# Kernel optimization log

Hardware: AMD Instinct MI355X
Metric: run time of the kernel (lower is better)

Reference implementation:

```python
import jax, jax.numpy as jnp
import numpy as np

B, S, D = 2, 4096, 2048
HQ, HK, HV = 32, 8, 8
H = max(HQ, HK, HV)
DK, DV = 64, 64
OUT = 2048
CHUNK = 64  # chunked-recurrent block size


def setup_inputs() -> dict:
    key = jax.random.key(0)
    k1, k2, k3 = jax.random.split(key, 3)
    x = jax.random.normal(k1, (B, S, D), dtype=jnp.float32)
    input_state = jnp.zeros((B, H * DK * DV), dtype=jnp.float32)
    qkv = HQ * DK + HK * DK + HV * DV  # 3072
    # Linear weights stored as [in, out]; equals torch weight.T so y = x @ W
    W_in = jax.random.normal(k2, (D, qkv), dtype=jnp.float32) * (D ** -0.5)
    W_out = jax.random.normal(k3, (H * DV, OUT), dtype=jnp.float32) * ((H * DV) ** -0.5)
    return {"x": x, "input_state": input_state, "W_in": W_in, "W_out": W_out}


def _linear_attention(q, k, v, S0):
    # q,k,v: [B,S,H,d]; S0: [B,H,DK,DV]
    nc = S // CHUNK
    # move chunk axis to front for lax.scan: [nc, B, CHUNK, H, d]
    qc = jnp.moveaxis(q.reshape(B, nc, CHUNK, H, DK), 1, 0)
    kc = jnp.moveaxis(k.reshape(B, nc, CHUNK, H, DK), 1, 0)
    vc = jnp.moveaxis(v.reshape(B, nc, CHUNK, H, DV), 1, 0)
    mask = jnp.tril(jnp.ones((CHUNK, CHUNK), dtype=bool))  # causal within chunk

    def step(Sstate, blk):
        qb, kb, vb = blk  # [B,C,H,d]
        A = jnp.einsum('bihd,bjhd->bhij', qb, kb)
        A = jnp.where(mask, A, jnp.zeros((), A.dtype))
        o = jnp.einsum('bhij,bjhd->bihd', A, vb) \
            + jnp.einsum('bihd,bhde->bihe', qb, Sstate)
        Sstate = Sstate + jnp.einsum('bjhd,bjhe->bhde', kb, vb)
        return Sstate, o

    Sf, o = jax.lax.scan(step, S0, (qc, kc, vc))
    o = jnp.moveaxis(o, 0, 1).reshape(B, S, H, DV)
    return o, Sf


def reference(x, input_state, W_in, W_out):
    proj = x @ W_in  # [B,S,3072]
    q, k, v = jnp.split(proj, [HQ * DK, HQ * DK + HK * DK], axis=-1)
    q = q.reshape(B, S, HQ, DK)
    k = k.reshape(B, S, HK, DK)
    v = v.reshape(B, S, HV, DV)
    # GQA: repeat kv heads up to num_heads = max(...)
    k = jnp.repeat(k, H // HK, axis=2)
    v = jnp.repeat(v, H // HV, axis=2)
    S0 = input_state.reshape(B, H, DK, DV)
    o, Sf = _linear_attention(q, k, v, S0)
    out = o.reshape(B, S, H * DV) @ W_out
    return out, Sf.reshape(B, H, DK * DV)
```

## Files before the change

kernel.cpp:

```cpp
#include <hip/hip_runtime.h>

typedef __bf16 bf16_t;
typedef __bf16 bf16x8 __attribute__((ext_vector_type(8)));
typedef __bf16 bf16x4 __attribute__((ext_vector_type(4)));
typedef float  f32x4  __attribute__((ext_vector_type(4)));

#define MFMA16(a,b,c) __builtin_amdgcn_mfma_f32_16x16x32_bf16((a),(b),(c),0,0,0)

__device__ __forceinline__ void gl_lds16(const void* g, void* l) {
    __builtin_amdgcn_global_load_lds(
        (__attribute__((address_space(1))) void*)(g),
        (__attribute__((address_space(3))) void*)(l),
        16, 0, 0);
}

static constexpr int S_TOT   = 8192;
static constexpr int D_IN    = 2048;
static constexpr int QKV     = 3072;
static constexpr int OUT_D   = 2048;
static constexpr int NCHUNK  = 64;

__global__ __launch_bounds__(256)
void cvt_f32_bf16(const float* __restrict__ in, bf16_t* __restrict__ out) {
    int i = blockIdx.x * 256 + threadIdx.x;
    f32x4 v = ((const f32x4*)in)[i];
    bf16x4 o;
    o[0] = (bf16_t)v[0]; o[1] = (bf16_t)v[1]; o[2] = (bf16_t)v[2]; o[3] = (bf16_t)v[3];
    ((bf16x4*)out)[i] = o;
}

__global__ __launch_bounds__(256)
void transpose_f32_bf16(const float* __restrict__ in, bf16_t* __restrict__ out, int R, int C) {
    __shared__ float tile[64][65];
    const int t  = threadIdx.x;
    const int r0 = blockIdx.y * 64, c0 = blockIdx.x * 64;
#pragma unroll
    for (int p = 0; p < 4; p++) {
        int row = p * 16 + (t >> 4);
        int col = (t & 15) * 4;
        f32x4 v = *(const f32x4*)&in[(size_t)(r0 + row) * C + c0 + col];
        tile[row][col + 0] = v[0]; tile[row][col + 1] = v[1];
        tile[row][col + 2] = v[2]; tile[row][col + 3] = v[3];
    }
    __syncthreads();
#pragma unroll
    for (int p = 0; p < 4; p++) {
        int oc  = p * 16 + (t >> 4);
        int orr = (t & 15) * 4;
        bf16x4 v;
        v[0] = (bf16_t)tile[orr + 0][oc]; v[1] = (bf16_t)tile[orr + 1][oc];
        v[2] = (bf16_t)tile[orr + 2][oc]; v[3] = (bf16_t)tile[orr + 3][oc];
        *(bf16x4*)&out[(size_t)(c0 + oc) * R + r0 + orr] = v;
    }
}

template<int OUT_BF16>
__global__ __launch_bounds__(256, 4)
void gemm_bt(const bf16_t* __restrict__ A, const bf16_t* __restrict__ Bt,
             void* __restrict__ Cout, int M, int N, int K) {
    __shared__ alignas(16) bf16_t lA[128 * 32];
    __shared__ alignas(16) bf16_t lB[128 * 32];
    const int tid = threadIdx.x;
    const int m0 = blockIdx.y * 128;
    const int n0 = blockIdx.x * 128;
    const int w = tid >> 6, lane = tid & 63;
    const int wr = (w >> 1) * 64, wc = (w & 1) * 64;
    const int l15 = lane & 15, q8 = (lane >> 4) * 8, q4 = (lane >> 4) * 4;
    f32x4 acc[4][4] = {};
    const bf16_t* Ag = A + (size_t)(m0 + (tid >> 2)) * K + (tid & 3) * 8;
    const bf16_t* Bg = Bt + (size_t)(n0 + (tid >> 2)) * K + (tid & 3) * 8;
    const size_t rowStep = (size_t)64 * K;
    bf16_t* lA_t = lA + tid * 8;
    bf16_t* lB_t = lB + tid * 8;
    for (int k0 = 0; k0 < K; k0 += 32) {
        gl_lds16(Ag + k0,           lA_t);
        gl_lds16(Ag + k0 + rowStep, lA_t + 64 * 32);
        gl_lds16(Bg + k0,           lB_t);
        gl_lds16(Bg + k0 + rowStep, lB_t + 64 * 32);
        __syncthreads();
        bf16x8 bfr[4];
#pragma unroll
        for (int nj = 0; nj < 4; nj++) bfr[nj] = *(const bf16x8*)&lB[(wc + nj * 16 + l15) * 32 + q8];
#pragma unroll
        for (int mi = 0; mi < 4; mi++) {
            bf16x8 afr = *(const bf16x8*)&lA[(wr + mi * 16 + l15) * 32 + q8];
#pragma unroll
            for (int nj = 0; nj < 4; nj++)
                acc[mi][nj] = MFMA16(afr, bfr[nj], acc[mi][nj]);
        }
        __syncthreads();
    }
    if (OUT_BF16) {
        bf16_t* C = (bf16_t*)Cout;
#pragma unroll
        for (int mi = 0; mi < 4; mi++)
#pragma unroll
            for (int nj = 0; nj < 4; nj++)
#pragma unroll
                for (int r = 0; r < 4; r++)
                    C[(size_t)(m0 + wr + mi * 16 + q4 + r) * N + n0 + wc + nj * 16 + l15] =
                        (bf16_t)acc[mi][nj][r];
    } else {
        float* C = (float*)Cout;
#pragma unroll
        for (int mi = 0; mi < 4; mi++)
#pragma unroll
            for (int nj = 0; nj < 4; nj++)
#pragma unroll
                for (int r = 0; r < 4; r++)
                    C[(size_t)(m0 + wr + mi * 16 + q4 + r) * N + n0 + wc + nj * 16 + l15] =
                        acc[mi][nj][r];
    }
}

__global__ __launch_bounds__(64)
void transpose_kv(const bf16_t* __restrict__ proj,
                  bf16_t* __restrict__ kT_g, bf16_t* __restrict__ vT_g) {
    const int idx = blockIdx.x;
    const int c = idx & 63, hk = (idx >> 6) & 7, b = idx >> 9;
    const int tokBase = b * 4096 + c * 64;
    __shared__ float tile[64][65];
    const int lane = threadIdx.x;
#pragma unroll
    for (int which = 0; which < 2; which++) {
        const bf16_t* src = proj + (size_t)tokBase * QKV + 2048 + which * 512 + hk * 64;
        bf16_t* dst = (which ? vT_g : kT_g) + (size_t)idx * 4096;
#pragma unroll
        for (int p = 0; p < 8; p++) {
            int tok = p * 8 + (lane >> 3);
            int d0  = (lane & 7) * 8;
            bf16x8 v = *(const bf16x8*)&src[(size_t)tok * QKV + d0];
#pragma unroll
            for (int e = 0; e < 8; e++) tile[tok][d0 + e] = (float)v[e];
        }
        __syncthreads();
#pragma unroll
        for (int p = 0; p < 8; p++) {
            int dk = p * 8 + (lane >> 3);
            int t0 = (lane & 7) * 8;
            bf16x8 o;
#pragma unroll
            for (int e = 0; e < 8; e++) o[e] = (bf16_t)tile[t0 + e][dk];
            *(bf16x8*)&dst[dk * 64 + t0] = o;
        }
        __syncthreads();
    }
}

__global__ __launch_bounds__(64)
void chunk_kv(const bf16_t* __restrict__ kT_g, const bf16_t* __restrict__ vT_g,
              float* __restrict__ Zc) {
    const int idx = blockIdx.x;
    const int lane = threadIdx.x;
    const int l15 = lane & 15, q8 = (lane >> 4) * 8, q4 = (lane >> 4) * 4;
    const bf16_t* vT = vT_g + (size_t)idx * 4096;
    const bf16_t* kT = kT_g + (size_t)idx * 4096;
    f32x4 acc[4][4] = {};
#pragma unroll
    for (int ks = 0; ks < 2; ks++) {
        bf16x8 af[4], bf_[4];
#pragma unroll
        for (int mi = 0; mi < 4; mi++) af[mi]  = *(const bf16x8*)&vT[(mi * 16 + l15) * 64 + ks * 32 + q8];
#pragma unroll
        for (int nj = 0; nj < 4; nj++) bf_[nj] = *(const bf16x8*)&kT[(nj * 16 + l15) * 64 + ks * 32 + q8];
#pragma unroll
        for (int mi = 0; mi < 4; mi++)
#pragma unroll
            for (int nj = 0; nj < 4; nj++)
                acc[mi][nj] = MFMA16(af[mi], bf_[nj], acc[mi][nj]);
    }
    float* zout = Zc + (size_t)idx * 4096;
#pragma unroll
    for (int mi = 0; mi < 4; mi++)
#pragma unroll
        for (int nj = 0; nj < 4; nj++)
#pragma unroll
            for (int r = 0; r < 4; r++)
                zout[(mi * 16 + q4 + r) * 64 + nj * 16 + l15] = acc[mi][nj][r];
}

__global__ __launch_bounds__(256)
void prefix_state(const float* __restrict__ Zc, const float* __restrict__ S0,
                  bf16_t* __restrict__ Zp, float* __restrict__ SfOut) {
    const int slice = blockIdx.x & 15;
    const int bh = blockIdx.x >> 4;
    const int h = bh & 31, b = bh >> 5;
    const int hk = h >> 2;
    const int e = slice * 256 + threadIdx.x;
    const int dv = e >> 6, dk = e & 63;
    float acc = S0[(size_t)b * 131072 + h * 4096 + dk * 64 + dv];
    const float* zc = Zc + ((size_t)(b * 8 + hk) * 64) * 4096 + e;
    bf16_t* zp = Zp + ((size_t)(b * 32 + h) * 64) * 4096 + e;
    for (int c = 0; c < NCHUNK; c++) {
        zp[(size_t)c * 4096] = (bf16_t)acc;
        acc += zc[(size_t)c * 4096];
    }
    SfOut[(size_t)b * 131072 + h * 4096 + dk * 64 + dv] = acc;
}

__global__ __launch_bounds__(64)
void attn_chunk(const bf16_t* __restrict__ proj, const bf16_t* __restrict__ vT_g,
                const bf16_t* __restrict__ Zp, bf16_t* __restrict__ O) {
    const int idx = blockIdx.x;
    const int g = idx & 3, hk = (idx >> 2) & 7, c = (idx >> 5) & 63, b = idx >> 11;
    const int h = hk * 4 + g;
    const int tokBase = b * 4096 + c * 64;
    __shared__ alignas(16) bf16_t zs[64 * 64];
    const int lane = threadIdx.x;
    const int l15 = lane & 15, q8 = (lane >> 4) * 8, q4 = (lane >> 4) * 4;
    const bf16_t* qrow  = proj + (size_t)tokBase * QKV + h * 64;
    const bf16_t* krow  = proj + (size_t)tokBase * QKV + 2048 + hk * 64;
    const bf16_t* zrow  = Zp + (((size_t)(b * 32 + h)) * 64 + c) * 4096;
    const bf16_t* vTrow = vT_g + ((size_t)(b * 8 + hk) * 64 + c) * 4096;

    bf16x8 qf[2][4];
#pragma unroll
    for (int ks = 0; ks < 2; ks++)
#pragma unroll
        for (int mi = 0; mi < 4; mi++)
            qf[ks][mi] = *(const bf16x8*)&qrow[(size_t)(mi * 16 + l15) * QKV + ks * 32 + q8];

    f32x4 oacc[4][4] = {};
#pragma unroll
    for (int ks = 0; ks < 2; ks++) {
        bf16x8 zf[4];
#pragma unroll
        for (int nj = 0; nj < 4; nj++) zf[nj] = *(const bf16x8*)&zrow[(nj * 16 + l15) * 64 + ks * 32 + q8];
#pragma unroll
        for (int mi = 0; mi < 4; mi++)
#pragma unroll
            for (int nj = 0; nj < 4; nj++)
                oacc[mi][nj] = MFMA16(qf[ks][mi], zf[nj], oacc[mi][nj]);
    }
    f32x4 sacc[4][4] = {};
#pragma unroll
    for (int ks = 0; ks < 2; ks++) {
        bf16x8 kf[4];
#pragma unroll
        for (int nj = 0; nj < 4; nj++) kf[nj] = *(const bf16x8*)&krow[(size_t)(nj * 16 + l15) * QKV + ks * 32 + q8];
#pragma unroll
        for (int mi = 0; mi < 4; mi++)
#pragma unroll
            for (int nj = 0; nj < 4; nj++)
                if (mi >= nj) sacc[mi][nj] = MFMA16(qf[ks][mi], kf[nj], sacc[mi][nj]);
    }
#pragma unroll
    for (int mi = 0; mi < 4; mi++)
#pragma unroll
        for (int nj = 0; nj < 4; nj++)
#pragma unroll
            for (int r = 0; r < 4; r++) {
                int ti = mi * 16 + q4 + r, tj = nj * 16 + l15;
                float v = (ti >= tj) ? sacc[mi][nj][r] : 0.0f;
                zs[ti * 64 + tj] = (bf16_t)v;
            }
    __syncthreads();
#pragma unroll
    for (int ks = 0; ks < 2; ks++) {
        bf16x8 sf[4], vf[4];
#pragma unroll
        for (int mi = 0; mi < 4; mi++) sf[mi] = *(const bf16x8*)&zs[(mi * 16 + l15) * 64 + ks * 32 + q8];
#pragma unroll
        for (int nj = 0; nj < 4; nj++) vf[nj] = *(const bf16x8*)&vTrow[(nj * 16 + l15) * 64 + ks * 32 + q8];
#pragma unroll
        for (int mi = 0; mi < 4; mi++)
#pragma unroll
            for (int nj = 0; nj < 4; nj++)
                oacc[mi][nj] = MFMA16(sf[mi], vf[nj], oacc[mi][nj]);
    }
    bf16_t* og = O + (size_t)tokBase * OUT_D + h * 64;
#pragma unroll
    for (int mi = 0; mi < 4; mi++)
#pragma unroll
        for (int nj = 0; nj < 4; nj++)
#pragma unroll
            for (int r = 0; r < 4; r++)
                og[(size_t)(mi * 16 + q4 + r) * OUT_D + nj * 16 + l15] = (bf16_t)oacc[mi][nj][r];
}

extern "C" void kernel_launch(void* const* d_in, const int* in_sizes, int n_in,
                              void* d_out, int out_size, void* d_ws, size_t ws_size,
                              hipStream_t stream) {
    const float* x     = (const float*)d_in[0];
    const float* S0    = (const float*)d_in[1];
    const float* W_in  = (const float*)d_in[2];
    const float* W_out = (const float*)d_in[3];

    char* ws = (char*)d_ws;
    bf16_t* xb    = (bf16_t*)(ws + 0);
    bf16_t* kT_g  = (bf16_t*)(ws + 16777216);
    bf16_t* WinT  = (bf16_t*)(ws + 33554432);
    bf16_t* vT_g  = (bf16_t*)(ws + 33554432);
    bf16_t* WoutT = (bf16_t*)(ws + 46137344);
    bf16_t* proj  = (bf16_t*)(ws + 54525952);
    float*  Zc    = (float*) (ws + 104857600);
    bf16_t* Zp    = (bf16_t*)(ws + 121634816);
    bf16_t* Ob    = (bf16_t*)(ws + 0);

    float* outMain  = (float*)d_out;
    float* outState = (float*)d_out + (size_t)S_TOT * OUT_D;

    cvt_f32_bf16<<<16384, 256, 0, stream>>>(x, xb);
    transpose_f32_bf16<<<dim3(48, 32), 256, 0, stream>>>(W_in, WinT, 2048, 3072);
    transpose_f32_bf16<<<dim3(32, 32), 256, 0, stream>>>(W_out, WoutT, 2048, 2048);
    gemm_bt<1><<<dim3(24, 64), 256, 0, stream>>>(xb, WinT, proj, S_TOT, QKV, D_IN);
    transpose_kv<<<1024, 64, 0, stream>>>(proj, kT_g, vT_g);
    chunk_kv<<<1024, 64, 0, stream>>>(kT_g, vT_g, Zc);
    prefix_state<<<1024, 256, 0, stream>>>(Zc, S0, Zp, outState);
    attn_chunk<<<4096, 64, 0, stream>>>(proj, vT_g, Zp, Ob);
    gemm_bt<0><<<dim3(16, 64), 256, 0, stream>>>(Ob, WoutT, outMain, S_TOT, OUT_D, OUT_D);
}
```

Before: 414.4 us.

## Fuse prep kernels, merge kv transpose with chunk state, regroup attention heads

Several changes land together. The three conversion and transpose kernels become one launch. The K/V transpose is fused with the per-chunk KᵀV computation, reading K directly from shared memory and dropping the kT buffer. The attention kernel now runs the four GQA query heads of a KV head as four warps in one 256-thread block, with a padded shared-memory stride to cut bank conflicts. The input GEMM processes two N tiles per block with half the grid. The intent is to reduce launch count, global traffic and LDS conflicts. The risks are lower GEMM parallelism and more LDS usage per block.

```diff
diff --git a/kernel.cpp b/kernel.cpp
--- a/kernel.cpp
+++ b/kernel.cpp
@@ -19,21 +19,28 @@
 static constexpr int QKV     = 3072;
 static constexpr int OUT_D   = 2048;
 static constexpr int NCHUNK  = 64;
+static constexpr int ZSTR    = 88;
 
 __global__ __launch_bounds__(256)
-void cvt_f32_bf16(const float* __restrict__ in, bf16_t* __restrict__ out) {
-    int i = blockIdx.x * 256 + threadIdx.x;
-    f32x4 v = ((const f32x4*)in)[i];
-    bf16x4 o;
-    o[0] = (bf16_t)v[0]; o[1] = (bf16_t)v[1]; o[2] = (bf16_t)v[2]; o[3] = (bf16_t)v[3];
-    ((bf16x4*)out)[i] = o;
-}
-
-__global__ __launch_bounds__(256)
-void transpose_f32_bf16(const float* __restrict__ in, bf16_t* __restrict__ out, int R, int C) {
+void prep(const float* __restrict__ x, bf16_t* __restrict__ xb,
+          const float* __restrict__ W_in, bf16_t* __restrict__ WinT,
+          const float* __restrict__ W_out, bf16_t* __restrict__ WoutT) {
     __shared__ float tile[64][65];
-    const int t  = threadIdx.x;
-    const int r0 = blockIdx.y * 64, c0 = blockIdx.x * 64;
+    const int bid = blockIdx.x;
+    const int t   = threadIdx.x;
+    if (bid < 16384) {
+        int i = bid * 256 + t;
+        f32x4 v = ((const f32x4*)x)[i];
+        bf16x4 o;
+        o[0] = (bf16_t)v[0]; o[1] = (bf16_t)v[1]; o[2] = (bf16_t)v[2]; o[3] = (bf16_t)v[3];
+        ((bf16x4*)xb)[i] = o;
+        return;
+    }
+    const float* in; bf16_t* out; int R, C, bx, by;
+    int tb = bid - 16384;
+    if (tb < 1536) { in = W_in;  out = WinT;  R = 2048; C = 3072; bx = tb % 48; by = tb / 48; }
+    else { tb -= 1536; in = W_out; out = WoutT; R = 2048; C = 2048; bx = tb % 32; by = tb / 32; }
+    const int r0 = by * 64, c0 = bx * 64;
 #pragma unroll
     for (int p = 0; p < 4; p++) {
         int row = p * 16 + (t >> 4);
@@ -54,7 +61,7 @@
     }
 }
 
-template<int OUT_BF16>
+template<int OUT_BF16, int NTILE, int NSTRIDE>
 __global__ __launch_bounds__(256, 4)
 void gemm_bt(const bf16_t* __restrict__ A, const bf16_t* __restrict__ Bt,
              void* __restrict__ Cout, int M, int N, int K) {
@@ -62,107 +69,106 @@
     __shared__ alignas(16) bf16_t lB[128 * 32];
     const int tid = threadIdx.x;
     const int m0 = blockIdx.y * 128;
-    const int n0 = blockIdx.x * 128;
     const int w = tid >> 6, lane = tid & 63;
     const int wr = (w >> 1) * 64, wc = (w & 1) * 64;
     const int l15 = lane & 15, q8 = (lane >> 4) * 8, q4 = (lane >> 4) * 4;
-    f32x4 acc[4][4] = {};
     const bf16_t* Ag = A + (size_t)(m0 + (tid >> 2)) * K + (tid & 3) * 8;
-    const bf16_t* Bg = Bt + (size_t)(n0 + (tid >> 2)) * K + (tid & 3) * 8;
     const size_t rowStep = (size_t)64 * K;
     bf16_t* lA_t = lA + tid * 8;
     bf16_t* lB_t = lB + tid * 8;
-    for (int k0 = 0; k0 < K; k0 += 32) {
-        gl_lds16(Ag + k0,           lA_t);
-        gl_lds16(Ag + k0 + rowStep, lA_t + 64 * 32);
-        gl_lds16(Bg + k0,           lB_t);
-        gl_lds16(Bg + k0 + rowStep, lB_t + 64 * 32);
-        __syncthreads();
-        bf16x8 bfr[4];
-#pragma unroll
-        for (int nj = 0; nj < 4; nj++) bfr[nj] = *(const bf16x8*)&lB[(wc + nj * 16 + l15) * 32 + q8];
-#pragma unroll
-        for (int mi = 0; mi < 4; mi++) {
-            bf16x8 afr = *(const bf16x8*)&lA[(wr + mi * 16 + l15) * 32 + q8];
-#pragma unroll
-            for (int nj = 0; nj < 4; nj++)
-                acc[mi][nj] = MFMA16(afr, bfr[nj], acc[mi][nj]);
+#pragma unroll
+    for (int tI = 0; tI < NTILE; tI++) {
+        const int n0 = (blockIdx.x + tI * NSTRIDE) * 128;
+        const bf16_t* Bg = Bt + (size_t)(n0 + (tid >> 2)) * K + (tid & 3) * 8;
+        f32x4 acc[4][4] = {};
+        for (int k0 = 0; k0 < K; k0 += 32) {
+            gl_lds16(Ag + k0,           lA_t);
+            gl_lds16(Ag + k0 + rowStep, lA_t + 64 * 32);
+            gl_lds16(Bg + k0,           lB_t);
+            gl_lds16(Bg + k0 + rowStep, lB_t + 64 * 32);
+            __syncthreads();
+            bf16x8 bfr[4];
+#pragma unroll
+            for (int nj = 0; nj < 4; nj++) bfr[nj] = *(const bf16x8*)&lB[(wc + nj * 16 + l15) * 32 + q8];
+#pragma unroll
+            for (int mi = 0; mi < 4; mi++) {
+                bf16x8 afr = *(const bf16x8*)&lA[(wr + mi * 16 + l15) * 32 + q8];
+#pragma unroll
+                for (int nj = 0; nj < 4; nj++)
+                    acc[mi][nj] = MFMA16(afr, bfr[nj], acc[mi][nj]);
+            }
+            __syncthreads();
         }
-        __syncthreads();
-    }
-    if (OUT_BF16) {
-        bf16_t* C = (bf16_t*)Cout;
-#pragma unroll
-        for (int mi = 0; mi < 4; mi++)
-#pragma unroll
-            for (int nj = 0; nj < 4; nj++)
-#pragma unroll
-                for (int r = 0; r < 4; r++)
-                    C[(size_t)(m0 + wr + mi * 16 + q4 + r) * N + n0 + wc + nj * 16 + l15] =
-                        (bf16_t)acc[mi][nj][r];
-    } else {
-        float* C = (float*)Cout;
-#pragma unroll
-        for (int mi = 0; mi < 4; mi++)
-#pragma unroll
-            for (int nj = 0; nj < 4; nj++)
-#pragma unroll
-                for (int r = 0; r < 4; r++)
-                    C[(size_t)(m0 + wr + mi * 16 + q4 + r) * N + n0 + wc + nj * 16 + l15] =
-                        acc[mi][nj][r];
+        if (OUT_BF16) {
+            bf16_t* C = (bf16_t*)Cout;
+#pragma unroll
+            for (int mi = 0; mi < 4; mi++)
+#pragma unroll
+                for (int nj = 0; nj < 4; nj++)
+#pragma unroll
+                    for (int r = 0; r < 4; r++)
+                        C[(size_t)(m0 + wr + mi * 16 + q4 + r) * N + n0 + wc + nj * 16 + l15] =
+                            (bf16_t)acc[mi][nj][r];
+        } else {
+            float* C = (float*)Cout;
+#pragma unroll
+            for (int mi = 0; mi < 4; mi++)
+#pragma unroll
+                for (int nj = 0; nj < 4; nj++)
+#pragma unroll
+                    for (int r = 0; r < 4; r++)
+                        C[(size_t)(m0 + wr + mi * 16 + q4 + r) * N + n0 + wc + nj * 16 + l15] =
+                            acc[mi][nj][r];
+        }
     }
 }
 
 __global__ __launch_bounds__(64)
-void transpose_kv(const bf16_t* __restrict__ proj,
-                  bf16_t* __restrict__ kT_g, bf16_t* __restrict__ vT_g) {
+void kv_fused(const bf16_t* __restrict__ proj, bf16_t* __restrict__ vT_g,
+              float* __restrict__ Zc) {
     const int idx = blockIdx.x;
     const int c = idx & 63, hk = (idx >> 6) & 7, b = idx >> 9;
     const int tokBase = b * 4096 + c * 64;
-    __shared__ float tile[64][65];
+    __shared__ float tk[64][65];
+    __shared__ float tv[64][65];
     const int lane = threadIdx.x;
-#pragma unroll
-    for (int which = 0; which < 2; which++) {
-        const bf16_t* src = proj + (size_t)tokBase * QKV + 2048 + which * 512 + hk * 64;
-        bf16_t* dst = (which ? vT_g : kT_g) + (size_t)idx * 4096;
-#pragma unroll
-        for (int p = 0; p < 8; p++) {
-            int tok = p * 8 + (lane >> 3);
-            int d0  = (lane & 7) * 8;
-            bf16x8 v = *(const bf16x8*)&src[(size_t)tok * QKV + d0];
-#pragma unroll
-            for (int e = 0; e < 8; e++) tile[tok][d0 + e] = (float)v[e];
+    const bf16_t* kg = proj + (size_t)tokBase * QKV + 2048 + hk * 64;
+    const bf16_t* vg = proj + (size_t)tokBase * QKV + 2560 + hk * 64;
+#pragma unroll
+    for (int p = 0; p < 8; p++) {
+        int tok = p * 8 + (lane >> 3);
+        int d0  = (lane & 7) * 8;
+        bf16x8 kv = *(const bf16x8*)&kg[(size_t)tok * QKV + d0];
+        bf16x8 vv = *(const bf16x8*)&vg[(size_t)tok * QKV + d0];
+#pragma unroll
+        for (int e = 0; e < 8; e++) {
+            tk[tok][d0 + e] = (float)kv[e];
+            tv[tok][d0 + e] = (float)vv[e];
         }
-        __syncthreads();
-#pragma unroll
-        for (int p = 0; p < 8; p++) {
-            int dk = p * 8 + (lane >> 3);
-            int t0 = (lane & 7) * 8;
-            bf16x8 o;
-#pragma unroll
-            for (int e = 0; e < 8; e++) o[e] = (bf16_t)tile[t0 + e][dk];
-            *(bf16x8*)&dst[dk * 64 + t0] = o;
-        }
-        __syncthreads();
-    }
-}
-
-__global__ __launch_bounds__(64)
-void chunk_kv(const bf16_t* __restrict__ kT_g, const bf16_t* __restrict__ vT_g,
-              float* __restrict__ Zc) {
-    const int idx = blockIdx.x;
-    const int lane = threadIdx.x;
+    }
+    __syncthreads();
+#pragma unroll
+    for (int p = 0; p < 8; p++) {
+        int dv = p * 8 + (lane >> 3);
+        int t0 = (lane & 7) * 8;
+        bf16x8 o;
+#pragma unroll
+        for (int e = 0; e < 8; e++) o[e] = (bf16_t)tv[t0 + e][dv];
+        *(bf16x8*)&vT_g[(size_t)idx * 4096 + dv * 64 + t0] = o;
+    }
     const int l15 = lane & 15, q8 = (lane >> 4) * 8, q4 = (lane >> 4) * 4;
-    const bf16_t* vT = vT_g + (size_t)idx * 4096;
-    const bf16_t* kT = kT_g + (size_t)idx * 4096;
     f32x4 acc[4][4] = {};
 #pragma unroll
     for (int ks = 0; ks < 2; ks++) {
         bf16x8 af[4], bf_[4];
 #pragma unroll
-        for (int mi = 0; mi < 4; mi++) af[mi]  = *(const bf16x8*)&vT[(mi * 16 + l15) * 64 + ks * 32 + q8];
-#pragma unroll
-        for (int nj = 0; nj < 4; nj++) bf_[nj] = *(const bf16x8*)&kT[(nj * 16 + l15) * 64 + ks * 32 + q8];
+        for (int mi = 0; mi < 4; mi++)
+#pragma unroll
+            for (int e = 0; e < 8; e++) af[mi][e] = (bf16_t)tv[ks * 32 + q8 + e][mi * 16 + l15];
+#pragma unroll
+        for (int nj = 0; nj < 4; nj++)
+#pragma unroll
+            for (int e = 0; e < 8; e++) bf_[nj][e] = (bf16_t)tk[ks * 32 + q8 + e][nj * 16 + l15];
 #pragma unroll
         for (int mi = 0; mi < 4; mi++)
 #pragma unroll
@@ -191,6 +197,7 @@
     float acc = S0[(size_t)b * 131072 + h * 4096 + dk * 64 + dv];
     const float* zc = Zc + ((size_t)(b * 8 + hk) * 64) * 4096 + e;
     bf16_t* zp = Zp + ((size_t)(b * 32 + h) * 64) * 4096 + e;
+#pragma unroll 4
     for (int c = 0; c < NCHUNK; c++) {
         zp[(size_t)c * 4096] = (bf16_t)acc;
         acc += zc[(size_t)c * 4096];
@@ -198,15 +205,16 @@
     SfOut[(size_t)b * 131072 + h * 4096 + dk * 64 + dv] = acc;
 }
 
-__global__ __launch_bounds__(64)
+__global__ __launch_bounds__(256)
 void attn_chunk(const bf16_t* __restrict__ proj, const bf16_t* __restrict__ vT_g,
                 const bf16_t* __restrict__ Zp, bf16_t* __restrict__ O) {
     const int idx = blockIdx.x;
-    const int g = idx & 3, hk = (idx >> 2) & 7, c = (idx >> 5) & 63, b = idx >> 11;
+    const int hk = idx & 7, c = (idx >> 3) & 63, b = idx >> 9;
+    const int g = threadIdx.x >> 6, lane = threadIdx.x & 63;
     const int h = hk * 4 + g;
     const int tokBase = b * 4096 + c * 64;
-    __shared__ alignas(16) bf16_t zs[64 * 64];
-    const int lane = threadIdx.x;
+    __shared__ alignas(16) bf16_t zs_all[4][64 * ZSTR];
+    bf16_t* zs = zs_all[g];
     const int l15 = lane & 15, q8 = (lane >> 4) * 8, q4 = (lane >> 4) * 4;
     const bf16_t* qrow  = proj + (size_t)tokBase * QKV + h * 64;
     const bf16_t* krow  = proj + (size_t)tokBase * QKV + 2048 + hk * 64;
@@ -252,14 +260,14 @@
             for (int r = 0; r < 4; r++) {
                 int ti = mi * 16 + q4 + r, tj = nj * 16 + l15;
                 float v = (ti >= tj) ? sacc[mi][nj][r] : 0.0f;
-                zs[ti * 64 + tj] = (bf16_t)v;
+                zs[ti * ZSTR + tj] = (bf16_t)v;
             }
     __syncthreads();
 #pragma unroll
     for (int ks = 0; ks < 2; ks++) {
         bf16x8 sf[4], vf[4];
 #pragma unroll
-        for (int mi = 0; mi < 4; mi++) sf[mi] = *(const bf16x8*)&zs[(mi * 16 + l15) * 64 + ks * 32 + q8];
+        for (int mi = 0; mi < 4; mi++) sf[mi] = *(const bf16x8*)&zs[(mi * 16 + l15) * ZSTR + ks * 32 + q8];
 #pragma unroll
         for (int nj = 0; nj < 4; nj++) vf[nj] = *(const bf16x8*)&vTrow[(nj * 16 + l15) * 64 + ks * 32 + q8];
 #pragma unroll
@@ -288,25 +296,21 @@
 
     char* ws = (char*)d_ws;
     bf16_t* xb    = (bf16_t*)(ws + 0);
-    bf16_t* kT_g  = (bf16_t*)(ws + 16777216);
     bf16_t* WinT  = (bf16_t*)(ws + 33554432);
-    bf16_t* vT_g  = (bf16_t*)(ws + 33554432);
     bf16_t* WoutT = (bf16_t*)(ws + 46137344);
     bf16_t* proj  = (bf16_t*)(ws + 54525952);
     float*  Zc    = (float*) (ws + 104857600);
     bf16_t* Zp    = (bf16_t*)(ws + 121634816);
-    bf16_t* Ob    = (bf16_t*)(ws + 0);
+    bf16_t* vT_g  = (bf16_t*)(ws + 0);
+    bf16_t* Ob    = (bf16_t*)(ws + 8388608);
 
     float* outMain  = (float*)d_out;
     float* outState = (float*)d_out + (size_t)S_TOT * OUT_D;
 
-    cvt_f32_bf16<<<16384, 256, 0, stream>>>(x, xb);
-    transpose_f32_bf16<<<dim3(48, 32), 256, 0, stream>>>(W_in, WinT, 2048, 3072);
-    transpose_f32_bf16<<<dim3(32, 32), 256, 0, stream>>>(W_out, WoutT, 2048, 2048);
-    gemm_bt<1><<<dim3(24, 64), 256, 0, stream>>>(xb, WinT, proj, S_TOT, QKV, D_IN);
-    transpose_kv<<<1024, 64, 0, stream>>>(proj, kT_g, vT_g);
-    chunk_kv<<<1024, 64, 0, stream>>>(kT_g, vT_g, Zc);
+    prep<<<16384 + 1536 + 1024, 256, 0, stream>>>(x, xb, W_in, WinT, W_out, WoutT);
+    gemm_bt<1, 2, 12><<<dim3(12, 64), 256, 0, stream>>>(xb, WinT, proj, S_TOT, QKV, D_IN);
+    kv_fused<<<1024, 64, 0, stream>>>(proj, vT_g, Zc);
     prefix_state<<<1024, 256, 0, stream>>>(Zc, S0, Zp, outState);
-    attn_chunk<<<4096, 64, 0, stream>>>(proj, vT_g, Zp, Ob);
-    gemm_bt<0><<<dim3(16, 64), 256, 0, stream>>>(Ob, WoutT, outMain, S_TOT, OUT_D, OUT_D);
-}
+    attn_chunk<<<1024, 256, 0, stream>>>(proj, vT_g, Zp, Ob);
+    gemm_bt<0, 1, 16><<<dim3(16, 64), 256, 0, stream>>>(Ob, WoutT, outMain, S_TOT, OUT_D, OUT_D);
+}
```

Result: slower. 423.1 us (+2.1%).
